# Optimization experiments

Measured on AMD Instinct MI355X. Metric: run time of the kernel, lower is better.

The kernel has to match this reference:

```python
import jax, jax.numpy as jnp
import numpy as np

T, K, D = 8192, 1024, 1024
START, STOP = K - 2, K - 1
NEG = -10000.0


def setup_inputs() -> dict:
    key = jax.random.key(0)
    ks = jax.random.split(key, 7)
    feats = jax.random.normal(ks[0], (T, K), jnp.float32)          # emission scores per utterance
    reps = jax.random.normal(ks[1], (T, D), jnp.float32)           # utterance representations (out_dict)
    spk_change = jax.random.randint(ks[2], (T,), 0, 2).astype(jnp.int32)  # speaker-change flag per step
    w_spk_change = jax.random.normal(ks[3], (2 * D,), jnp.float32)
    w_spk_unchange = jax.random.normal(ks[4], (2 * D,), jnp.float32)
    ti = jax.random.normal(ks[5], (K, K), jnp.float32)
    ta = jax.random.normal(ks[6], (K, K), jnp.float32)
    # CRF constraint init: nothing transitions INTO START, nothing transitions FROM STOP
    ti = ti.at[START, :].set(NEG).at[:, STOP].set(NEG)
    ta = ta.at[START, :].set(NEG).at[:, STOP].set(NEG)
    return dict(feats=feats, reps=reps, w_spk_change=w_spk_change,
                w_spk_unchange=w_spk_unchange, transitions_inter=ti,
                transitions_intra=ta, spk_change=spk_change)


def reference(feats, reps, w_spk_change, w_spk_unchange,
              transitions_inter, transitions_intra, spk_change):
    T_, K_ = feats.shape
    # concat(repr[i-1], repr[i]); at i==0 the code duplicates repr[0]
    prev = jnp.concatenate([reps[:1], reps[:-1]], axis=0)          # [T, D]
    cat = jnp.concatenate([prev, reps], axis=1)                    # [T, 2D]
    a_change = jax.nn.sigmoid(cat @ w_spk_change)                  # [T]
    a_unchange = jax.nn.sigmoid(cat @ w_spk_unchange)              # [T]
    # i==0 or same speaker -> unchange gate; speaker change (i>0) -> change gate
    use_change = spk_change.astype(bool) & (jnp.arange(T_) > 0)
    gate = jnp.where(use_change, a_change, a_unchange)             # [T]

    init = jnp.full((K_,), NEG, jnp.float32).at[START].set(0.0)

    def step(fv, xs):
        feat, g = xs                                               # feat: [K], g: scalar
        trans = g * transitions_inter + (1.0 - g) * transitions_intra  # [K_next, K_prev]
        # next_tag_var[next, prev] = fv[prev] + trans[next, prev] + emit[next]
        fv_new = jax.nn.logsumexp(fv[None, :] + trans + feat[:, None], axis=1)
        return fv_new, None

    fv, _ = jax.lax.scan(step, init, (feats, gate))

    # terminal: unchange gate on duplicated last representation, STOP row
    cat_last = jnp.concatenate([reps[-1], reps[-1]])               # [2D]
    g_t = jax.nn.sigmoid(cat_last @ w_spk_unchange)
    terminal = fv + g_t * transitions_inter[STOP] + (1.0 - g_t) * transitions_intra[STOP]
    return jax.nn.logsumexp(terminal)                              # log partition (scalar)
```

## Files before the change

kernel.cpp:

```cpp
#include <hip/hip_runtime.h>
#include <stdint.h>

#define T_STEPS 8192
#define K_TAGS 1024
#define D_DIM 1024
#define START_TAG 1022
#define STOP_TAG 1023
#define NEGV (-10000.0f)
#define LOG2E 1.4426950408889634f
#define LN2 0.6931471805599453f

#define NBLK 256
#define ROWS_PB 4
#define C8 8

__device__ __forceinline__ unsigned long long ld_agent_u64(const unsigned long long* p) {
  return __hip_atomic_load(p, __ATOMIC_RELAXED, __HIP_MEMORY_SCOPE_AGENT);
}
__device__ __forceinline__ void st_agent_u64(unsigned long long* p, unsigned long long v) {
  __hip_atomic_store(p, v, __ATOMIC_RELAXED, __HIP_MEMORY_SCOPE_AGENT);
}

__global__ void init_ws_kernel(unsigned long long* fvbuf, int* bmax) {
  int i = blockIdx.x * blockDim.x + threadIdx.x;
  if (i < 2 * K_TAGS) fvbuf[i] = 0ull;
  if (i == 0) *bmax = 0;
}

__global__ __launch_bounds__(256) void gate_kernel(
    const float* __restrict__ reps, const float* __restrict__ wc,
    const float* __restrict__ wu, const int* __restrict__ spk,
    float* __restrict__ gate, float* __restrict__ g_term) {
  const int gw = (int)((blockIdx.x * blockDim.x + threadIdx.x) >> 6);
  const int lane = threadIdx.x & 63;
  if (gw > T_STEPS) return;
  const int tcur = (gw < T_STEPS) ? gw : (T_STEPS - 1);
  const int tprv = (gw < T_STEPS) ? (gw > 0 ? gw - 1 : 0) : (T_STEPS - 1);
  const float* cur = reps + (size_t)tcur * D_DIM;
  const float* prv = reps + (size_t)tprv * D_DIM;
  float sc = 0.f, su = 0.f;
#pragma unroll
  for (int c = 0; c < 4; ++c) {
    const int d = lane * 4 + c * 256;
    float4 rp = *(const float4*)(prv + d);
    float4 rc = *(const float4*)(cur + d);
    float4 w1 = *(const float4*)(wc + d);
    float4 w2 = *(const float4*)(wc + D_DIM + d);
    float4 w3 = *(const float4*)(wu + d);
    float4 w4 = *(const float4*)(wu + D_DIM + d);
    sc += rp.x * w1.x + rp.y * w1.y + rp.z * w1.z + rp.w * w1.w;
    sc += rc.x * w2.x + rc.y * w2.y + rc.z * w2.z + rc.w * w2.w;
    su += rp.x * w3.x + rp.y * w3.y + rp.z * w3.z + rp.w * w3.w;
    su += rc.x * w4.x + rc.y * w4.y + rc.z * w4.z + rc.w * w4.w;
  }
#pragma unroll
  for (int off = 32; off; off >>= 1) {
    sc += __shfl_xor(sc, off);
    su += __shfl_xor(su, off);
  }
  if (lane == 0) {
    if (gw < T_STEPS) {
      bool uc = (gw > 0) && (spk[gw] != 0);
      float x = uc ? sc : su;
      gate[gw] = 1.0f / (1.0f + __expf(-x));
    } else {
      *g_term = 1.0f / (1.0f + __expf(-su));
    }
  }
}

__global__ __launch_bounds__(256) void bmax_kernel(
    const float* __restrict__ ti, const float* __restrict__ ta, int* bmax) {
  size_t i = (size_t)blockIdx.x * blockDim.x + threadIdx.x;
  size_t n = (size_t)K_TAGS * K_TAGS;
  float m = 0.f;
  for (size_t j = i; j < n; j += (size_t)gridDim.x * blockDim.x)
    m = fmaxf(m, fmaxf(ti[j], ta[j]));
#pragma unroll
  for (int off = 32; off; off >>= 1) m = fmaxf(m, __shfl_xor(m, off));
  if ((threadIdx.x & 63) == 0) atomicMax(bmax, __float_as_int(m));
}

__global__ __launch_bounds__(256) void crf_kernel(
    const float* __restrict__ feats, const float* __restrict__ ti,
    const float* __restrict__ ta, const float* __restrict__ gate,
    const float* __restrict__ g_term_p, const int* __restrict__ bmax_p,
    unsigned long long* fvbuf, float* __restrict__ out) {
  const int b = blockIdx.x;
  const int tid = threadIdx.x;
  const int lane = tid & 63;
  const int w = tid >> 6;
  const int r = b * ROWS_PB + w;
  const int e0 = tid * 4;

  __shared__ __align__(16) float fvs[2][K_TAGS];
  __shared__ float wredM[4];
  __shared__ float wredS[4];

  float ta2[16], df2[16];
  {
    const float2* taP = reinterpret_cast<const float2*>(ta + (size_t)r * K_TAGS) + lane;
    const float2* tiP = reinterpret_cast<const float2*>(ti + (size_t)r * K_TAGS) + lane;
#pragma unroll
    for (int c = 0; c < C8; ++c) {
      float2 a = taP[64 * c];
      float2 i_ = tiP[64 * c];
      ta2[2 * c] = a.x * LOG2E;
      df2[2 * c] = (i_.x - a.x) * LOG2E;
      ta2[2 * c + 1] = a.y * LOG2E;
      df2[2 * c + 1] = (i_.y - a.y) * LOG2E;
    }
  }
  const float bmax2 = __int_as_float(*bmax_p) * LOG2E;

  if (tid < ROWS_PB) {
    int rr = b * ROWS_PB + tid;
    float v = (rr == START_TAG) ? 0.0f : NEGV * LOG2E;
    st_agent_u64(&fvbuf[rr],
                 (1ull << 32) | (unsigned long long)__float_as_uint(v));
  }

  for (int t = 0; t < T_STEPS; ++t) {
    const int slot = t & 1;
    const unsigned want = (unsigned)(t + 1);
    const float g = gate[t];
    float featv = 0.f;
    if (lane == 0) featv = feats[(size_t)t * K_TAGS + r];

    unsigned long long* ep = &fvbuf[slot * K_TAGS + e0];
    unsigned long long u0 = ld_agent_u64(ep + 0);
    unsigned long long u1 = ld_agent_u64(ep + 1);
    unsigned long long u2 = ld_agent_u64(ep + 2);
    unsigned long long u3 = ld_agent_u64(ep + 3);
    while ((unsigned)(u0 >> 32) < want || (unsigned)(u1 >> 32) < want ||
           (unsigned)(u2 >> 32) < want || (unsigned)(u3 >> 32) < want) {
      u0 = ld_agent_u64(ep + 0);
      u1 = ld_agent_u64(ep + 1);
      u2 = ld_agent_u64(ep + 2);
      u3 = ld_agent_u64(ep + 3);
    }
    const float v0 = __uint_as_float((unsigned)u0);
    const float v1 = __uint_as_float((unsigned)u1);
    const float v2 = __uint_as_float((unsigned)u2);
    const float v3 = __uint_as_float((unsigned)u3);

    *reinterpret_cast<float4*>(&fvs[slot][e0]) = make_float4(v0, v1, v2, v3);
    float m = fmaxf(fmaxf(v0, v1), fmaxf(v2, v3));
#pragma unroll
    for (int off = 32; off; off >>= 1) m = fmaxf(m, __shfl_xor(m, off));
    if (lane == 0) wredM[w] = m;
    __syncthreads();
    const float M2 =
        fmaxf(fmaxf(wredM[0], wredM[1]), fmaxf(wredM[2], wredM[3])) + bmax2;

    float acc = 0.f;
    const float2* fp = reinterpret_cast<const float2*>(&fvs[slot][0]) + lane;
#pragma unroll
    for (int c = 0; c < C8; ++c) {
      float2 f = fp[64 * c];
      acc += exp2f(__builtin_fmaf(g, df2[2 * c], ta2[2 * c]) + (f.x - M2));
      acc += exp2f(__builtin_fmaf(g, df2[2 * c + 1], ta2[2 * c + 1]) + (f.y - M2));
    }
#pragma unroll
    for (int off = 32; off; off >>= 1) acc += __shfl_xor(acc, off);

    if (lane == 0) {
      float fvnew = M2 + __log2f(acc) + featv * LOG2E;
      st_agent_u64(&fvbuf[(slot ^ 1) * K_TAGS + r],
                   ((unsigned long long)(unsigned)(t + 2) << 32) |
                       (unsigned long long)__float_as_uint(fvnew));
    }
  }

  if (b == 0) {
    const unsigned want = (unsigned)(T_STEPS + 1);
    unsigned long long* ep = &fvbuf[(T_STEPS & 1) * K_TAGS + e0];
    unsigned long long u0 = ld_agent_u64(ep + 0);
    unsigned long long u1 = ld_agent_u64(ep + 1);
    unsigned long long u2 = ld_agent_u64(ep + 2);
    unsigned long long u3 = ld_agent_u64(ep + 3);
    while ((unsigned)(u0 >> 32) < want || (unsigned)(u1 >> 32) < want ||
           (unsigned)(u2 >> 32) < want || (unsigned)(u3 >> 32) < want) {
      u0 = ld_agent_u64(ep + 0);
      u1 = ld_agent_u64(ep + 1);
      u2 = ld_agent_u64(ep + 2);
      u3 = ld_agent_u64(ep + 3);
    }
    const float gt = *g_term_p;
    float term[4];
    const unsigned long long uu[4] = {u0, u1, u2, u3};
#pragma unroll
    for (int j = 0; j < 4; ++j) {
      const int k = e0 + j;
      float tis = ti[(size_t)STOP_TAG * K_TAGS + k];
      float tas = ta[(size_t)STOP_TAG * K_TAGS + k];
      term[j] = __uint_as_float((unsigned)uu[j]) +
                (tas + gt * (tis - tas)) * LOG2E;
    }
    float m = fmaxf(fmaxf(term[0], term[1]), fmaxf(term[2], term[3]));
#pragma unroll
    for (int off = 32; off; off >>= 1) m = fmaxf(m, __shfl_xor(m, off));
    if (lane == 0) wredM[w] = m;
    __syncthreads();
    const float M2 = fmaxf(fmaxf(wredM[0], wredM[1]), fmaxf(wredM[2], wredM[3]));
    float e = exp2f(term[0] - M2) + exp2f(term[1] - M2) +
              exp2f(term[2] - M2) + exp2f(term[3] - M2);
#pragma unroll
    for (int off = 32; off; off >>= 1) e += __shfl_xor(e, off);
    if (lane == 0) wredS[w] = e;
    __syncthreads();
    if (tid == 0) {
      float s = wredS[0] + wredS[1] + wredS[2] + wredS[3];
      out[0] = (M2 + __log2f(s)) * LN2;
    }
  }
}

extern "C" void kernel_launch(void* const* d_in, const int* in_sizes, int n_in,
                              void* d_out, int out_size, void* d_ws, size_t ws_size,
                              hipStream_t stream) {
  (void)in_sizes; (void)n_in; (void)out_size; (void)ws_size;
  const float* feats = (const float*)d_in[0];
  const float* reps  = (const float*)d_in[1];
  const float* wc    = (const float*)d_in[2];
  const float* wu    = (const float*)d_in[3];
  const float* ti    = (const float*)d_in[4];
  const float* ta    = (const float*)d_in[5];
  const int*   spk   = (const int*)d_in[6];
  float* out = (float*)d_out;

  unsigned long long* fvbuf = (unsigned long long*)d_ws;
  float* gate  = (float*)((char*)d_ws + 2 * K_TAGS * sizeof(unsigned long long));
  float* gterm = gate + T_STEPS;
  int*   bmax  = (int*)(gterm + 1);

  init_ws_kernel<<<dim3(8), dim3(256), 0, stream>>>(fvbuf, bmax);
  gate_kernel<<<dim3((T_STEPS + 1 + 3) / 4), dim3(256), 0, stream>>>(
      reps, wc, wu, spk, gate, gterm);
  bmax_kernel<<<dim3(512), dim3(256), 0, stream>>>(ti, ta, bmax);
  crf_kernel<<<dim3(NBLK), dim3(256), 0, stream>>>(feats, ti, ta, gate, gterm,
                                                   bmax, fvbuf, out);
}
```

Baseline: 15.66 ms.

## Pack step tag into float low bits and use fewer, larger CRF blocks

The cross-block handshake now carries a 32-bit value whose low 8 mantissa bits hold the step tag, replacing the 64-bit value+counter words. Each thread polls one word with a short sleep between polls. The grid shrinks from 256 blocks of 256 threads to 64 blocks of 1024 threads, so fewer blocks take part in the per-step exchange. The intent is to cut the latency and traffic of the global barrier on the serial recurrence, at the cost of slight precision loss from the truncated mantissa, a clamp on very negative scores, and a wrapping 8-bit tag.

New measurement: 30.50 ms. 1.95x slower.

```diff
diff --git a/kernel.cpp b/kernel.cpp
--- a/kernel.cpp
+++ b/kernel.cpp
@@ -9,21 +9,25 @@
 #define NEGV (-10000.0f)
 #define LOG2E 1.4426950408889634f
 #define LN2 0.6931471805599453f
-
-#define NBLK 256
-#define ROWS_PB 4
+#define CLAMP2 (-1.0e5f)
+
+#define NBLK 64
+#define ROWS_PB 16
 #define C8 8
 
-__device__ __forceinline__ unsigned long long ld_agent_u64(const unsigned long long* p) {
+__device__ __forceinline__ unsigned ld_agent_u32(const unsigned* p) {
   return __hip_atomic_load(p, __ATOMIC_RELAXED, __HIP_MEMORY_SCOPE_AGENT);
 }
-__device__ __forceinline__ void st_agent_u64(unsigned long long* p, unsigned long long v) {
+__device__ __forceinline__ void st_agent_u32(unsigned* p, unsigned v) {
   __hip_atomic_store(p, v, __ATOMIC_RELAXED, __HIP_MEMORY_SCOPE_AGENT);
 }
-
-__global__ void init_ws_kernel(unsigned long long* fvbuf, int* bmax) {
+__device__ __forceinline__ unsigned tag_pack(float v, unsigned tag8) {
+  return (__float_as_uint(v) & ~0xFFu) | tag8;
+}
+
+__global__ void init_ws_kernel(unsigned* fvbuf, int* bmax) {
   int i = blockIdx.x * blockDim.x + threadIdx.x;
-  if (i < 2 * K_TAGS) fvbuf[i] = 0ull;
+  if (i < 2 * K_TAGS) fvbuf[i] = 0xFFu;
   if (i == 0) *bmax = 0;
 }
 
@@ -81,21 +85,20 @@
   if ((threadIdx.x & 63) == 0) atomicMax(bmax, __float_as_int(m));
 }
 
-__global__ __launch_bounds__(256) void crf_kernel(
+__global__ __launch_bounds__(1024) void crf_kernel(
     const float* __restrict__ feats, const float* __restrict__ ti,
     const float* __restrict__ ta, const float* __restrict__ gate,
     const float* __restrict__ g_term_p, const int* __restrict__ bmax_p,
-    unsigned long long* fvbuf, float* __restrict__ out) {
+    unsigned* fvb, float* __restrict__ out) {
   const int b = blockIdx.x;
   const int tid = threadIdx.x;
   const int lane = tid & 63;
   const int w = tid >> 6;
   const int r = b * ROWS_PB + w;
-  const int e0 = tid * 4;
 
   __shared__ __align__(16) float fvs[2][K_TAGS];
-  __shared__ float wredM[4];
-  __shared__ float wredS[4];
+  __shared__ __align__(16) float wredM[2][16];
+  __shared__ float wredS[16];
 
   float ta2[16], df2[16];
   {
@@ -116,42 +119,39 @@
   if (tid < ROWS_PB) {
     int rr = b * ROWS_PB + tid;
     float v = (rr == START_TAG) ? 0.0f : NEGV * LOG2E;
-    st_agent_u64(&fvbuf[rr],
-                 (1ull << 32) | (unsigned long long)__float_as_uint(v));
+    st_agent_u32(&fvb[rr], tag_pack(v, 0u));
   }
 
   for (int t = 0; t < T_STEPS; ++t) {
     const int slot = t & 1;
-    const unsigned want = (unsigned)(t + 1);
+    const unsigned want = (unsigned)(t & 0xFF);
     const float g = gate[t];
     float featv = 0.f;
     if (lane == 0) featv = feats[(size_t)t * K_TAGS + r];
 
-    unsigned long long* ep = &fvbuf[slot * K_TAGS + e0];
-    unsigned long long u0 = ld_agent_u64(ep + 0);
-    unsigned long long u1 = ld_agent_u64(ep + 1);
-    unsigned long long u2 = ld_agent_u64(ep + 2);
-    unsigned long long u3 = ld_agent_u64(ep + 3);
-    while ((unsigned)(u0 >> 32) < want || (unsigned)(u1 >> 32) < want ||
-           (unsigned)(u2 >> 32) < want || (unsigned)(u3 >> 32) < want) {
-      u0 = ld_agent_u64(ep + 0);
-      u1 = ld_agent_u64(ep + 1);
-      u2 = ld_agent_u64(ep + 2);
-      u3 = ld_agent_u64(ep + 3);
-    }
-    const float v0 = __uint_as_float((unsigned)u0);
-    const float v1 = __uint_as_float((unsigned)u1);
-    const float v2 = __uint_as_float((unsigned)u2);
-    const float v3 = __uint_as_float((unsigned)u3);
-
-    *reinterpret_cast<float4*>(&fvs[slot][e0]) = make_float4(v0, v1, v2, v3);
-    float m = fmaxf(fmaxf(v0, v1), fmaxf(v2, v3));
+    unsigned* ep = &fvb[slot * K_TAGS + tid];
+    unsigned u = ld_agent_u32(ep);
+    while ((u & 0xFFu) != want) {
+      __builtin_amdgcn_s_sleep(1);
+      u = ld_agent_u32(ep);
+    }
+    const float v = __uint_as_float(u);
+
+    fvs[slot][tid] = v;
+    float m = v;
 #pragma unroll
     for (int off = 32; off; off >>= 1) m = fmaxf(m, __shfl_xor(m, off));
-    if (lane == 0) wredM[w] = m;
+    if (lane == 0) wredM[slot][w] = m;
     __syncthreads();
-    const float M2 =
-        fmaxf(fmaxf(wredM[0], wredM[1]), fmaxf(wredM[2], wredM[3])) + bmax2;
+    float4 m0 = *reinterpret_cast<const float4*>(&wredM[slot][0]);
+    float4 m1 = *reinterpret_cast<const float4*>(&wredM[slot][4]);
+    float4 m2 = *reinterpret_cast<const float4*>(&wredM[slot][8]);
+    float4 m3 = *reinterpret_cast<const float4*>(&wredM[slot][12]);
+    float mm = fmaxf(fmaxf(fmaxf(m0.x, m0.y), fmaxf(m0.z, m0.w)),
+                     fmaxf(fmaxf(m1.x, m1.y), fmaxf(m1.z, m1.w)));
+    mm = fmaxf(mm, fmaxf(fmaxf(fmaxf(m2.x, m2.y), fmaxf(m2.z, m2.w)),
+                         fmaxf(fmaxf(m3.x, m3.y), fmaxf(m3.z, m3.w))));
+    const float M2 = mm + bmax2;
 
     float acc = 0.f;
     const float2* fp = reinterpret_cast<const float2*>(&fvs[slot][0]) + lane;
@@ -165,53 +165,43 @@
     for (int off = 32; off; off >>= 1) acc += __shfl_xor(acc, off);
 
     if (lane == 0) {
-      float fvnew = M2 + __log2f(acc) + featv * LOG2E;
-      st_agent_u64(&fvbuf[(slot ^ 1) * K_TAGS + r],
-                   ((unsigned long long)(unsigned)(t + 2) << 32) |
-                       (unsigned long long)__float_as_uint(fvnew));
+      float fvnew = fmaxf(M2 + __log2f(acc) + featv * LOG2E, CLAMP2);
+      st_agent_u32(&fvb[(slot ^ 1) * K_TAGS + r],
+                   tag_pack(fvnew, (unsigned)((t + 1) & 0xFF)));
     }
   }
 
   if (b == 0) {
-    const unsigned want = (unsigned)(T_STEPS + 1);
-    unsigned long long* ep = &fvbuf[(T_STEPS & 1) * K_TAGS + e0];
-    unsigned long long u0 = ld_agent_u64(ep + 0);
-    unsigned long long u1 = ld_agent_u64(ep + 1);
-    unsigned long long u2 = ld_agent_u64(ep + 2);
-    unsigned long long u3 = ld_agent_u64(ep + 3);
-    while ((unsigned)(u0 >> 32) < want || (unsigned)(u1 >> 32) < want ||
-           (unsigned)(u2 >> 32) < want || (unsigned)(u3 >> 32) < want) {
-      u0 = ld_agent_u64(ep + 0);
-      u1 = ld_agent_u64(ep + 1);
-      u2 = ld_agent_u64(ep + 2);
-      u3 = ld_agent_u64(ep + 3);
-    }
+    const unsigned want = (unsigned)(T_STEPS & 0xFF);
     const float gt = *g_term_p;
-    float term[4];
-    const unsigned long long uu[4] = {u0, u1, u2, u3};
-#pragma unroll
-    for (int j = 0; j < 4; ++j) {
-      const int k = e0 + j;
-      float tis = ti[(size_t)STOP_TAG * K_TAGS + k];
-      float tas = ta[(size_t)STOP_TAG * K_TAGS + k];
-      term[j] = __uint_as_float((unsigned)uu[j]) +
-                (tas + gt * (tis - tas)) * LOG2E;
-    }
-    float m = fmaxf(fmaxf(term[0], term[1]), fmaxf(term[2], term[3]));
+    const float tis = ti[(size_t)STOP_TAG * K_TAGS + tid];
+    const float tas = ta[(size_t)STOP_TAG * K_TAGS + tid];
+    unsigned* ep = &fvb[(T_STEPS & 1) * K_TAGS + tid];
+    unsigned u = ld_agent_u32(ep);
+    while ((u & 0xFFu) != want) {
+      __builtin_amdgcn_s_sleep(1);
+      u = ld_agent_u32(ep);
+    }
+    const float term2 = __uint_as_float(u) + (tas + gt * (tis - tas)) * LOG2E;
+
+    float m = term2;
 #pragma unroll
     for (int off = 32; off; off >>= 1) m = fmaxf(m, __shfl_xor(m, off));
-    if (lane == 0) wredM[w] = m;
+    if (lane == 0) wredM[0][w] = m;
     __syncthreads();
-    const float M2 = fmaxf(fmaxf(wredM[0], wredM[1]), fmaxf(wredM[2], wredM[3]));
-    float e = exp2f(term[0] - M2) + exp2f(term[1] - M2) +
-              exp2f(term[2] - M2) + exp2f(term[3] - M2);
+    float mm = wredM[0][0];
+#pragma unroll
+    for (int i = 1; i < 16; ++i) mm = fmaxf(mm, wredM[0][i]);
+    float e = exp2f(term2 - mm);
 #pragma unroll
     for (int off = 32; off; off >>= 1) e += __shfl_xor(e, off);
     if (lane == 0) wredS[w] = e;
     __syncthreads();
     if (tid == 0) {
-      float s = wredS[0] + wredS[1] + wredS[2] + wredS[3];
-      out[0] = (M2 + __log2f(s)) * LN2;
+      float s = 0.f;
+#pragma unroll
+      for (int i = 0; i < 16; ++i) s += wredS[i];
+      out[0] = (mm + __log2f(s)) * LN2;
     }
   }
 }
@@ -229,8 +219,8 @@
   const int*   spk   = (const int*)d_in[6];
   float* out = (float*)d_out;
 
-  unsigned long long* fvbuf = (unsigned long long*)d_ws;
-  float* gate  = (float*)((char*)d_ws + 2 * K_TAGS * sizeof(unsigned long long));
+  unsigned* fvbuf = (unsigned*)d_ws;
+  float* gate  = (float*)((char*)d_ws + 2 * K_TAGS * sizeof(unsigned));
   float* gterm = gate + T_STEPS;
   int*   bmax  = (int*)(gterm + 1);
 
@@ -238,6 +228,6 @@
   gate_kernel<<<dim3((T_STEPS + 1 + 3) / 4), dim3(256), 0, stream>>>(
       reps, wc, wu, spk, gate, gterm);
   bmax_kernel<<<dim3(512), dim3(256), 0, stream>>>(ti, ta, bmax);
-  crf_kernel<<<dim3(NBLK), dim3(256), 0, stream>>>(feats, ti, ta, gate, gterm,
-                                                   bmax, fvbuf, out);
-}
+  crf_kernel<<<dim3(NBLK), dim3(1024), 0, stream>>>(feats, ti, ta, gate, gterm,
+                                                    bmax, fvbuf, out);
+}
```

## Use lagged block max with margin to take reduction off the critical path

Applied to the files above, without the earlier changes.

The logsumexp shift now comes from the previous step's per-warp maxima plus a fixed margin, instead of a fresh max reduction each step. That reduction moves after the store of the new forward value, so it overlaps the wait for the next step. The spin-wait loop also keeps two loads of the flags in flight at once, and the exp accumulation is split into two independent chains. The risk is numerical: if the forward values jump by more than the margin between steps, the shifted exponents could overflow or underflow.

Result: no change. 15.93 ms (+1.7%).

```diff
diff --git a/kernel.cpp b/kernel.cpp
--- a/kernel.cpp
+++ b/kernel.cpp
@@ -9,10 +9,13 @@
 #define NEGV (-10000.0f)
 #define LOG2E 1.4426950408889634f
 #define LN2 0.6931471805599453f
+#define MARGIN2 40.0f
 
 #define NBLK 256
 #define ROWS_PB 4
 #define C8 8
+
+#define TAG(u) ((unsigned)((u) >> 32))
 
 __device__ __forceinline__ unsigned long long ld_agent_u64(const unsigned long long* p) {
   return __hip_atomic_load(p, __ATOMIC_RELAXED, __HIP_MEMORY_SCOPE_AGENT);
@@ -94,7 +97,7 @@
   const int e0 = tid * 4;
 
   __shared__ __align__(16) float fvs[2][K_TAGS];
-  __shared__ float wredM[4];
+  __shared__ __align__(16) float wredM[2][4];
   __shared__ float wredS[4];
 
   float ta2[16], df2[16];
@@ -113,6 +116,8 @@
   }
   const float bmax2 = __int_as_float(*bmax_p) * LOG2E;
 
+  if (tid < 8) wredM[tid >> 2][tid & 3] = 0.0f;
+
   if (tid < ROWS_PB) {
     int rr = b * ROWS_PB + tid;
     float v = (rr == START_TAG) ? 0.0f : NEGV * LOG2E;
@@ -128,48 +133,50 @@
     if (lane == 0) featv = feats[(size_t)t * K_TAGS + r];
 
     unsigned long long* ep = &fvbuf[slot * K_TAGS + e0];
-    unsigned long long u0 = ld_agent_u64(ep + 0);
-    unsigned long long u1 = ld_agent_u64(ep + 1);
-    unsigned long long u2 = ld_agent_u64(ep + 2);
-    unsigned long long u3 = ld_agent_u64(ep + 3);
-    while ((unsigned)(u0 >> 32) < want || (unsigned)(u1 >> 32) < want ||
-           (unsigned)(u2 >> 32) < want || (unsigned)(u3 >> 32) < want) {
-      u0 = ld_agent_u64(ep + 0);
-      u1 = ld_agent_u64(ep + 1);
-      u2 = ld_agent_u64(ep + 2);
-      u3 = ld_agent_u64(ep + 3);
-    }
-    const float v0 = __uint_as_float((unsigned)u0);
-    const float v1 = __uint_as_float((unsigned)u1);
-    const float v2 = __uint_as_float((unsigned)u2);
-    const float v3 = __uint_as_float((unsigned)u3);
+    unsigned long long a0 = ld_agent_u64(ep + 0), a1 = ld_agent_u64(ep + 1),
+                       a2 = ld_agent_u64(ep + 2), a3 = ld_agent_u64(ep + 3);
+    unsigned long long b0 = ld_agent_u64(ep + 0), b1 = ld_agent_u64(ep + 1),
+                       b2 = ld_agent_u64(ep + 2), b3 = ld_agent_u64(ep + 3);
+    while (TAG(a0) < want || TAG(a1) < want || TAG(a2) < want || TAG(a3) < want) {
+      a0 = b0; a1 = b1; a2 = b2; a3 = b3;
+      b0 = ld_agent_u64(ep + 0); b1 = ld_agent_u64(ep + 1);
+      b2 = ld_agent_u64(ep + 2); b3 = ld_agent_u64(ep + 3);
+    }
+    const float v0 = __uint_as_float((unsigned)a0);
+    const float v1 = __uint_as_float((unsigned)a1);
+    const float v2 = __uint_as_float((unsigned)a2);
+    const float v3 = __uint_as_float((unsigned)a3);
 
     *reinterpret_cast<float4*>(&fvs[slot][e0]) = make_float4(v0, v1, v2, v3);
-    float m = fmaxf(fmaxf(v0, v1), fmaxf(v2, v3));
-#pragma unroll
-    for (int off = 32; off; off >>= 1) m = fmaxf(m, __shfl_xor(m, off));
-    if (lane == 0) wredM[w] = m;
     __syncthreads();
-    const float M2 =
-        fmaxf(fmaxf(wredM[0], wredM[1]), fmaxf(wredM[2], wredM[3])) + bmax2;
-
-    float acc = 0.f;
+
+    const float4 mp = *reinterpret_cast<const float4*>(&wredM[slot ^ 1][0]);
+    const float shift =
+        fmaxf(fmaxf(mp.x, mp.y), fmaxf(mp.z, mp.w)) + bmax2 + MARGIN2;
+
+    float acc0 = 0.f, acc1 = 0.f;
     const float2* fp = reinterpret_cast<const float2*>(&fvs[slot][0]) + lane;
 #pragma unroll
     for (int c = 0; c < C8; ++c) {
       float2 f = fp[64 * c];
-      acc += exp2f(__builtin_fmaf(g, df2[2 * c], ta2[2 * c]) + (f.x - M2));
-      acc += exp2f(__builtin_fmaf(g, df2[2 * c + 1], ta2[2 * c + 1]) + (f.y - M2));
-    }
+      acc0 += exp2f(__builtin_fmaf(g, df2[2 * c], ta2[2 * c]) + (f.x - shift));
+      acc1 += exp2f(__builtin_fmaf(g, df2[2 * c + 1], ta2[2 * c + 1]) + (f.y - shift));
+    }
+    float acc = acc0 + acc1;
 #pragma unroll
     for (int off = 32; off; off >>= 1) acc += __shfl_xor(acc, off);
 
     if (lane == 0) {
-      float fvnew = M2 + __log2f(acc) + featv * LOG2E;
+      float fvnew = shift + __log2f(acc) + featv * LOG2E;
       st_agent_u64(&fvbuf[(slot ^ 1) * K_TAGS + r],
                    ((unsigned long long)(unsigned)(t + 2) << 32) |
                        (unsigned long long)__float_as_uint(fvnew));
     }
+
+    float lm = fmaxf(fmaxf(v0, v1), fmaxf(v2, v3));
+#pragma unroll
+    for (int off = 32; off; off >>= 1) lm = fmaxf(lm, __shfl_xor(lm, off));
+    if (lane == 0) wredM[slot][w] = lm;
   }
 
   if (b == 0) {
@@ -179,8 +186,7 @@
     unsigned long long u1 = ld_agent_u64(ep + 1);
     unsigned long long u2 = ld_agent_u64(ep + 2);
     unsigned long long u3 = ld_agent_u64(ep + 3);
-    while ((unsigned)(u0 >> 32) < want || (unsigned)(u1 >> 32) < want ||
-           (unsigned)(u2 >> 32) < want || (unsigned)(u3 >> 32) < want) {
+    while (TAG(u0) < want || TAG(u1) < want || TAG(u2) < want || TAG(u3) < want) {
       u0 = ld_agent_u64(ep + 0);
       u1 = ld_agent_u64(ep + 1);
       u2 = ld_agent_u64(ep + 2);
@@ -200,9 +206,10 @@
     float m = fmaxf(fmaxf(term[0], term[1]), fmaxf(term[2], term[3]));
 #pragma unroll
     for (int off = 32; off; off >>= 1) m = fmaxf(m, __shfl_xor(m, off));
-    if (lane == 0) wredM[w] = m;
+    if (lane == 0) wredM[0][w] = m;
     __syncthreads();
-    const float M2 = fmaxf(fmaxf(wredM[0], wredM[1]), fmaxf(wredM[2], wredM[3]));
+    const float M2 = fmaxf(fmaxf(wredM[0][0], wredM[0][1]),
+                           fmaxf(wredM[0][2], wredM[0][3]));
     float e = exp2f(term[0] - M2) + exp2f(term[1] - M2) +
               exp2f(term[2] - M2) + exp2f(term[3] - M2);
 #pragma unroll
```

## Use one wavefront per CRF row with DPP reductions and exact per-step max

Applied to the files above, without the earlier changes.

The persistent CRF kernel goes from 256 blocks of four wavefronts to 1024 single-wavefront blocks, one per tag row. Each wave loads all 1024 previous forward values straight from the global flag buffer. This removes the shared-memory staging, the __syncthreads and the cross-wave reduction on every step. Reductions switch from shuffles to DPP row operations with readlane. The global transition max precompute kernel is dropped in favour of the exact per-step max of the forward vector. The next step's emission is prefetched, and the terminal step reuses the STOP row held in registers. The cost is 1024 co-resident spinning blocks, each issuing sixteen 64-bit polling loads per lane, which adds L2 traffic and needs every block resident at once to avoid deadlock.

New measurement: 54.59 ms. 3.49x slower.

```diff
diff --git a/kernel.cpp b/kernel.cpp
--- a/kernel.cpp
+++ b/kernel.cpp
@@ -10,21 +10,46 @@
 #define LOG2E 1.4426950408889634f
 #define LN2 0.6931471805599453f
 
-#define NBLK 256
-#define ROWS_PB 4
-#define C8 8
-
-__device__ __forceinline__ unsigned long long ld_agent_u64(const unsigned long long* p) {
+#define NBLK 1024
+#define TAG(u) ((unsigned)((u) >> 32))
+
+static __device__ __forceinline__ unsigned long long ld_agent_u64(
+    const unsigned long long* p) {
   return __hip_atomic_load(p, __ATOMIC_RELAXED, __HIP_MEMORY_SCOPE_AGENT);
 }
-__device__ __forceinline__ void st_agent_u64(unsigned long long* p, unsigned long long v) {
+static __device__ __forceinline__ void st_agent_u64(unsigned long long* p,
+                                                    unsigned long long v) {
   __hip_atomic_store(p, v, __ATOMIC_RELAXED, __HIP_MEMORY_SCOPE_AGENT);
 }
 
-__global__ void init_ws_kernel(unsigned long long* fvbuf, int* bmax) {
+template <int CTRL>
+static __device__ __forceinline__ float dpp_mov(float x, float old) {
+  return __int_as_float(__builtin_amdgcn_update_dpp(
+      __float_as_int(old), __float_as_int(x), CTRL, 0xF, 0xF, false));
+}
+static __device__ __forceinline__ float wave_red_max63(float x) {
+  const float NI = -3.0e38f;
+  x = fmaxf(x, dpp_mov<0x111>(x, NI));
+  x = fmaxf(x, dpp_mov<0x112>(x, NI));
+  x = fmaxf(x, dpp_mov<0x114>(x, NI));
+  x = fmaxf(x, dpp_mov<0x118>(x, NI));
+  x = fmaxf(x, dpp_mov<0x142>(x, NI));
+  x = fmaxf(x, dpp_mov<0x143>(x, NI));
+  return x;
+}
+static __device__ __forceinline__ float wave_red_sum63(float x) {
+  x += dpp_mov<0x111>(x, 0.0f);
+  x += dpp_mov<0x112>(x, 0.0f);
+  x += dpp_mov<0x114>(x, 0.0f);
+  x += dpp_mov<0x118>(x, 0.0f);
+  x += dpp_mov<0x142>(x, 0.0f);
+  x += dpp_mov<0x143>(x, 0.0f);
+  return x;
+}
+
+__global__ void init_ws_kernel(unsigned long long* fvbuf) {
   int i = blockIdx.x * blockDim.x + threadIdx.x;
   if (i < 2 * K_TAGS) fvbuf[i] = 0ull;
-  if (i == 0) *bmax = 0;
 }
 
 __global__ __launch_bounds__(256) void gate_kernel(
@@ -69,150 +94,114 @@
   }
 }
 
-__global__ __launch_bounds__(256) void bmax_kernel(
-    const float* __restrict__ ti, const float* __restrict__ ta, int* bmax) {
-  size_t i = (size_t)blockIdx.x * blockDim.x + threadIdx.x;
-  size_t n = (size_t)K_TAGS * K_TAGS;
-  float m = 0.f;
-  for (size_t j = i; j < n; j += (size_t)gridDim.x * blockDim.x)
-    m = fmaxf(m, fmaxf(ti[j], ta[j]));
-#pragma unroll
-  for (int off = 32; off; off >>= 1) m = fmaxf(m, __shfl_xor(m, off));
-  if ((threadIdx.x & 63) == 0) atomicMax(bmax, __float_as_int(m));
-}
-
-__global__ __launch_bounds__(256) void crf_kernel(
+__global__ __launch_bounds__(64) void crf_kernel(
     const float* __restrict__ feats, const float* __restrict__ ti,
     const float* __restrict__ ta, const float* __restrict__ gate,
-    const float* __restrict__ g_term_p, const int* __restrict__ bmax_p,
-    unsigned long long* fvbuf, float* __restrict__ out) {
-  const int b = blockIdx.x;
-  const int tid = threadIdx.x;
-  const int lane = tid & 63;
-  const int w = tid >> 6;
-  const int r = b * ROWS_PB + w;
-  const int e0 = tid * 4;
-
-  __shared__ __align__(16) float fvs[2][K_TAGS];
-  __shared__ float wredM[4];
-  __shared__ float wredS[4];
+    const float* __restrict__ g_term_p, unsigned long long* fvb,
+    float* __restrict__ out) {
+  const int r = blockIdx.x;
+  const int lane = threadIdx.x;
 
   float ta2[16], df2[16];
   {
-    const float2* taP = reinterpret_cast<const float2*>(ta + (size_t)r * K_TAGS) + lane;
-    const float2* tiP = reinterpret_cast<const float2*>(ti + (size_t)r * K_TAGS) + lane;
-#pragma unroll
-    for (int c = 0; c < C8; ++c) {
-      float2 a = taP[64 * c];
-      float2 i_ = tiP[64 * c];
-      ta2[2 * c] = a.x * LOG2E;
-      df2[2 * c] = (i_.x - a.x) * LOG2E;
-      ta2[2 * c + 1] = a.y * LOG2E;
-      df2[2 * c + 1] = (i_.y - a.y) * LOG2E;
-    }
-  }
-  const float bmax2 = __int_as_float(*bmax_p) * LOG2E;
-
-  if (tid < ROWS_PB) {
-    int rr = b * ROWS_PB + tid;
-    float v = (rr == START_TAG) ? 0.0f : NEGV * LOG2E;
-    st_agent_u64(&fvbuf[rr],
+    const float* taR = ta + (size_t)r * K_TAGS + lane;
+    const float* tiR = ti + (size_t)r * K_TAGS + lane;
+#pragma unroll
+    for (int c = 0; c < 16; ++c) {
+      float a = taR[64 * c];
+      float i_ = tiR[64 * c];
+      ta2[c] = a * LOG2E;
+      df2[c] = (i_ - a) * LOG2E;
+    }
+  }
+
+  if (lane == 0) {
+    float v = (r == START_TAG) ? 0.0f : NEGV * LOG2E;
+    st_agent_u64(&fvb[r],
                  (1ull << 32) | (unsigned long long)__float_as_uint(v));
   }
+
+  float featv = (lane == 63) ? feats[r] : 0.0f;
 
   for (int t = 0; t < T_STEPS; ++t) {
     const int slot = t & 1;
     const unsigned want = (unsigned)(t + 1);
     const float g = gate[t];
-    float featv = 0.f;
-    if (lane == 0) featv = feats[(size_t)t * K_TAGS + r];
-
-    unsigned long long* ep = &fvbuf[slot * K_TAGS + e0];
-    unsigned long long u0 = ld_agent_u64(ep + 0);
-    unsigned long long u1 = ld_agent_u64(ep + 1);
-    unsigned long long u2 = ld_agent_u64(ep + 2);
-    unsigned long long u3 = ld_agent_u64(ep + 3);
-    while ((unsigned)(u0 >> 32) < want || (unsigned)(u1 >> 32) < want ||
-           (unsigned)(u2 >> 32) < want || (unsigned)(u3 >> 32) < want) {
-      u0 = ld_agent_u64(ep + 0);
-      u1 = ld_agent_u64(ep + 1);
-      u2 = ld_agent_u64(ep + 2);
-      u3 = ld_agent_u64(ep + 3);
-    }
-    const float v0 = __uint_as_float((unsigned)u0);
-    const float v1 = __uint_as_float((unsigned)u1);
-    const float v2 = __uint_as_float((unsigned)u2);
-    const float v3 = __uint_as_float((unsigned)u3);
-
-    *reinterpret_cast<float4*>(&fvs[slot][e0]) = make_float4(v0, v1, v2, v3);
-    float m = fmaxf(fmaxf(v0, v1), fmaxf(v2, v3));
-#pragma unroll
-    for (int off = 32; off; off >>= 1) m = fmaxf(m, __shfl_xor(m, off));
-    if (lane == 0) wredM[w] = m;
-    __syncthreads();
-    const float M2 =
-        fmaxf(fmaxf(wredM[0], wredM[1]), fmaxf(wredM[2], wredM[3])) + bmax2;
-
-    float acc = 0.f;
-    const float2* fp = reinterpret_cast<const float2*>(&fvs[slot][0]) + lane;
-#pragma unroll
-    for (int c = 0; c < C8; ++c) {
-      float2 f = fp[64 * c];
-      acc += exp2f(__builtin_fmaf(g, df2[2 * c], ta2[2 * c]) + (f.x - M2));
-      acc += exp2f(__builtin_fmaf(g, df2[2 * c + 1], ta2[2 * c + 1]) + (f.y - M2));
-    }
-#pragma unroll
-    for (int off = 32; off; off >>= 1) acc += __shfl_xor(acc, off);
-
-    if (lane == 0) {
-      float fvnew = M2 + __log2f(acc) + featv * LOG2E;
-      st_agent_u64(&fvbuf[(slot ^ 1) * K_TAGS + r],
+
+    unsigned long long* ep = &fvb[slot * K_TAGS + lane];
+    unsigned long long u[16];
+    for (;;) {
+      unsigned bad = 0;
+#pragma unroll
+      for (int c = 0; c < 16; ++c) u[c] = ld_agent_u64(ep + 64 * c);
+#pragma unroll
+      for (int c = 0; c < 16; ++c) bad |= (unsigned)(TAG(u[c]) < want);
+      if (!__any((int)bad)) break;
+    }
+
+    float featv_next = 0.0f;
+    if (lane == 63 && t + 1 < T_STEPS)
+      featv_next = feats[(size_t)(t + 1) * K_TAGS + r];
+
+    float fv[16];
+#pragma unroll
+    for (int c = 0; c < 16; ++c) fv[c] = __uint_as_float((unsigned)u[c]);
+
+    float m = fv[0];
+#pragma unroll
+    for (int c = 1; c < 16; ++c) m = fmaxf(m, fv[c]);
+    m = wave_red_max63(m);
+    const float sh =
+        __int_as_float(__builtin_amdgcn_readlane(__float_as_int(m), 63));
+
+    float a0 = 0.f, a1 = 0.f, a2 = 0.f, a3 = 0.f;
+#pragma unroll
+    for (int c = 0; c < 16; c += 4) {
+      a0 += exp2f(__builtin_fmaf(g, df2[c + 0], ta2[c + 0]) + (fv[c + 0] - sh));
+      a1 += exp2f(__builtin_fmaf(g, df2[c + 1], ta2[c + 1]) + (fv[c + 1] - sh));
+      a2 += exp2f(__builtin_fmaf(g, df2[c + 2], ta2[c + 2]) + (fv[c + 2] - sh));
+      a3 += exp2f(__builtin_fmaf(g, df2[c + 3], ta2[c + 3]) + (fv[c + 3] - sh));
+    }
+    float acc = wave_red_sum63((a0 + a1) + (a2 + a3));
+
+    if (lane == 63) {
+      float fvnew = sh + __log2f(acc) + featv * LOG2E;
+      st_agent_u64(&fvb[(slot ^ 1) * K_TAGS + r],
                    ((unsigned long long)(unsigned)(t + 2) << 32) |
                        (unsigned long long)__float_as_uint(fvnew));
     }
-  }
-
-  if (b == 0) {
+    featv = featv_next;
+  }
+
+  if (r == STOP_TAG) {
     const unsigned want = (unsigned)(T_STEPS + 1);
-    unsigned long long* ep = &fvbuf[(T_STEPS & 1) * K_TAGS + e0];
-    unsigned long long u0 = ld_agent_u64(ep + 0);
-    unsigned long long u1 = ld_agent_u64(ep + 1);
-    unsigned long long u2 = ld_agent_u64(ep + 2);
-    unsigned long long u3 = ld_agent_u64(ep + 3);
-    while ((unsigned)(u0 >> 32) < want || (unsigned)(u1 >> 32) < want ||
-           (unsigned)(u2 >> 32) < want || (unsigned)(u3 >> 32) < want) {
-      u0 = ld_agent_u64(ep + 0);
-      u1 = ld_agent_u64(ep + 1);
-      u2 = ld_agent_u64(ep + 2);
-      u3 = ld_agent_u64(ep + 3);
+    unsigned long long* ep = &fvb[(T_STEPS & 1) * K_TAGS + lane];
+    unsigned long long u[16];
+    for (;;) {
+      unsigned bad = 0;
+#pragma unroll
+      for (int c = 0; c < 16; ++c) u[c] = ld_agent_u64(ep + 64 * c);
+#pragma unroll
+      for (int c = 0; c < 16; ++c) bad |= (unsigned)(TAG(u[c]) < want);
+      if (!__any((int)bad)) break;
     }
     const float gt = *g_term_p;
-    float term[4];
-    const unsigned long long uu[4] = {u0, u1, u2, u3};
-#pragma unroll
-    for (int j = 0; j < 4; ++j) {
-      const int k = e0 + j;
-      float tis = ti[(size_t)STOP_TAG * K_TAGS + k];
-      float tas = ta[(size_t)STOP_TAG * K_TAGS + k];
-      term[j] = __uint_as_float((unsigned)uu[j]) +
-                (tas + gt * (tis - tas)) * LOG2E;
-    }
-    float m = fmaxf(fmaxf(term[0], term[1]), fmaxf(term[2], term[3]));
-#pragma unroll
-    for (int off = 32; off; off >>= 1) m = fmaxf(m, __shfl_xor(m, off));
-    if (lane == 0) wredM[w] = m;
-    __syncthreads();
-    const float M2 = fmaxf(fmaxf(wredM[0], wredM[1]), fmaxf(wredM[2], wredM[3]));
-    float e = exp2f(term[0] - M2) + exp2f(term[1] - M2) +
-              exp2f(term[2] - M2) + exp2f(term[3] - M2);
-#pragma unroll
-    for (int off = 32; off; off >>= 1) e += __shfl_xor(e, off);
-    if (lane == 0) wredS[w] = e;
-    __syncthreads();
-    if (tid == 0) {
-      float s = wredS[0] + wredS[1] + wredS[2] + wredS[3];
-      out[0] = (M2 + __log2f(s)) * LN2;
-    }
+    float v[16];
+#pragma unroll
+    for (int c = 0; c < 16; ++c)
+      v[c] = __uint_as_float((unsigned)u[c]) +
+             __builtin_fmaf(gt, df2[c], ta2[c]);
+    float m = v[0];
+#pragma unroll
+    for (int c = 1; c < 16; ++c) m = fmaxf(m, v[c]);
+    m = wave_red_max63(m);
+    const float M =
+        __int_as_float(__builtin_amdgcn_readlane(__float_as_int(m), 63));
+    float e = 0.f;
+#pragma unroll
+    for (int c = 0; c < 16; ++c) e += exp2f(v[c] - M);
+    e = wave_red_sum63(e);
+    if (lane == 63) out[0] = (M + __log2f(e)) * LN2;
   }
 }
 
@@ -232,12 +221,10 @@
   unsigned long long* fvbuf = (unsigned long long*)d_ws;
   float* gate  = (float*)((char*)d_ws + 2 * K_TAGS * sizeof(unsigned long long));
   float* gterm = gate + T_STEPS;
-  int*   bmax  = (int*)(gterm + 1);
-
-  init_ws_kernel<<<dim3(8), dim3(256), 0, stream>>>(fvbuf, bmax);
+
+  init_ws_kernel<<<dim3(8), dim3(256), 0, stream>>>(fvbuf);
   gate_kernel<<<dim3((T_STEPS + 1 + 3) / 4), dim3(256), 0, stream>>>(
       reps, wc, wu, spk, gate, gterm);
-  bmax_kernel<<<dim3(512), dim3(256), 0, stream>>>(ti, ta, bmax);
-  crf_kernel<<<dim3(NBLK), dim3(256), 0, stream>>>(feats, ti, ta, gate, gterm,
-                                                   bmax, fvbuf, out);
-}
+  crf_kernel<<<dim3(NBLK), dim3(64), 0, stream>>>(feats, ti, ta, gate, gterm,
+                                                  fvbuf, out);
+}
```
